# Kernel optimization log

Measured on AMD Instinct MI355X. Metric: run time of the kernel, lower is better.

## Reference

```python
import jax, jax.numpy as jnp
import numpy as np

N = 100            # node_num
B = 8              # batch
H = 256            # node_feature_hidden_dim
FD, FL = 16, 16    # node_feature_dim, node_feature_len
OUT = 4            # edge_output_dim
E = N * (N - 1)    # 9900 directed edges (off-diagonal)
_off = np.ones((N, N)) - np.eye(N)
REC, SEND = np.where(_off)   # rel_rec one-hot rows = REC, rel_send = SEND
REC = jnp.asarray(REC, jnp.int32)
SEND = jnp.asarray(SEND, jnp.int32)
BN_EPS = 1e-5


def _mlp(x, w1, b1, w2, b2, g, beta):
    # Linear-ReLU-Linear-ReLU-BatchNorm1d (training-mode batch stats, dropout=0)
    h = jax.nn.relu(x @ w1 + b1)
    h = jax.nn.relu(h @ w2 + b2)
    b_, e_, f_ = h.shape
    hf = h.reshape(b_ * e_, f_)
    mu = hf.mean(0)
    var = hf.var(0)  # biased variance, as torch BN uses for normalization
    hn = (hf - mu) * jax.lax.rsqrt(var + BN_EPS) * g + beta
    return hn.reshape(b_, e_, f_)


def _node2edge(x):
    # gather form of rel_send @ x / rel_rec @ x, cat([senders, receivers])
    return jnp.concatenate([x[:, SEND, :], x[:, REC, :]], axis=2)


def _edge2node(x):
    # scatter form of rel_rec.T @ x; original divides by incoming.size(1) == N
    incoming = jnp.zeros((x.shape[0], N, x.shape[2]), x.dtype).at[:, REC, :].add(x)
    return incoming / N


def setup_inputs() -> dict:
    key = jax.random.key(0)
    ks = jax.random.split(key, 40)

    def rn(k, shape, s=0.05):
        return (jax.random.normal(k, shape) * s).astype(jnp.float32)

    inp = {
        'x': rn(ks[0], (B, N, FD, FL), 1.0),
        'h': rn(ks[1], (B, N, 8, 8), 1.0),
        't_nodes': N,
        't_edges': E,
        'nodes_mask': jnp.ones((N,), jnp.int32),
        'edges_mask': jnp.ones((E,), jnp.int32),
    }
    n_in = {'mlp1': FD * FL, 'mlp2': 2 * H, 'mlp3': H, 'mlp4': 3 * H}
    i = 2
    for name, nin in n_in.items():
        inp[name + '_w1'] = rn(ks[i], (nin, H)); i += 1
        inp[name + '_b1'] = jnp.full((H,), 0.1, jnp.float32)
        inp[name + '_w2'] = rn(ks[i], (H, H)); i += 1
        inp[name + '_b2'] = jnp.full((H,), 0.1, jnp.float32)
        inp[name + '_g'] = jnp.ones((H,), jnp.float32)
        inp[name + '_beta'] = jnp.zeros((H,), jnp.float32)
    inp['fc_w'] = rn(ks[i], (H, OUT)); i += 1
    inp['fc_b'] = jnp.full((OUT,), 0.1, jnp.float32)
    return inp


def reference(x, h, t_nodes, t_edges, nodes_mask, edges_mask,
              mlp1_w1, mlp1_b1, mlp1_w2, mlp1_b2, mlp1_g, mlp1_beta,
              mlp2_w1, mlp2_b1, mlp2_w2, mlp2_b2, mlp2_g, mlp2_beta,
              mlp3_w1, mlp3_b1, mlp3_w2, mlp3_b2, mlp3_g, mlp3_beta,
              mlp4_w1, mlp4_b1, mlp4_w2, mlp4_b2, mlp4_g, mlp4_beta,
              fc_w, fc_b):
    # h, t_nodes, t_edges, nodes_mask, edges_mask are unused by the original forward
    xx = x.reshape(x.shape[0], x.shape[1], -1).astype(jnp.float32)  # [B,N,FD*FL]
    xx = _mlp(xx, mlp1_w1, mlp1_b1, mlp1_w2, mlp1_b2, mlp1_g, mlp1_beta)  # [B,N,H]
    xe = _node2edge(xx)                                                   # [B,E,2H]
    xe = _mlp(xe, mlp2_w1, mlp2_b1, mlp2_w2, mlp2_b2, mlp2_g, mlp2_beta)  # [B,E,H]
    x_skip = xe
    xn = _edge2node(xe)                                                   # [B,N,H]
    xn = _mlp(xn, mlp3_w1, mlp3_b1, mlp3_w2, mlp3_b2, mlp3_g, mlp3_beta)
    xe2 = _node2edge(xn)                                                  # [B,E,2H]
    xc = jnp.concatenate([xe2, x_skip], axis=2)                           # [B,E,3H]
    xc = _mlp(xc, mlp4_w1, mlp4_b1, mlp4_w2, mlp4_b2, mlp4_g, mlp4_beta)  # [B,E,H]
    z_g = xc @ fc_w + fc_b                                                # [B,E,OUT]
    return z_g
```

## Files before the change

kernel.cpp:

```cpp
#include <hip/hip_runtime.h>
#include <hip/hip_bf16.h>

#define Nn 100
#define Bb 8
#define Hh 256
#define Ee 9900
#define RE 79200
#define RN 800
#define BN_EPS 1e-5f

typedef __attribute__((ext_vector_type(8))) unsigned short ushort8_t;
typedef __attribute__((ext_vector_type(4))) unsigned short ushort4_t;
typedef __attribute__((ext_vector_type(8))) short bf16x8;
typedef __attribute__((ext_vector_type(4))) float f32x4;

__device__ __forceinline__ float bf2f(unsigned short u){
  return __uint_as_float(((unsigned)u) << 16);
}
__device__ __forceinline__ unsigned short f2bf(float f){
  unsigned u = __float_as_uint(f);
  return (unsigned short)((u + 0x7fffu + ((u >> 16) & 1u)) >> 16);
}

__device__ __forceinline__ void affine_prologue(const float* __restrict__ stats,
    float cnt, const float* __restrict__ g, const float* __restrict__ beta,
    float* a, float* c, int tid){
  if (tid < 256){
    float inv = 1.0f / cnt;
    float mu  = stats[tid] * inv;
    float var = fmaxf(stats[256 + tid] * inv - mu * mu, 0.f);
    float aa  = g[tid] * rsqrtf(var + BN_EPS);
    a[tid] = aa;
    c[tid] = beta[tid] - mu * aa;
  }
}

__device__ __forceinline__ void affine_reg(const float* __restrict__ stats,
    float cnt, const float* __restrict__ g, const float* __restrict__ be,
    int cb, float4& av, float4& cv){
  float4 s = *(const float4*)(stats + cb);
  float4 q = *(const float4*)(stats + 256 + cb);
  float4 gg = *(const float4*)(g + cb);
  float4 bb = *(const float4*)(be + cb);
  float inv = 1.0f / cnt;
  float mx = s.x*inv, my = s.y*inv, mz = s.z*inv, mw = s.w*inv;
  av.x = gg.x * rsqrtf(fmaxf(q.x*inv - mx*mx, 0.f) + BN_EPS); cv.x = bb.x - mx*av.x;
  av.y = gg.y * rsqrtf(fmaxf(q.y*inv - my*my, 0.f) + BN_EPS); cv.y = bb.y - my*av.y;
  av.z = gg.z * rsqrtf(fmaxf(q.z*inv - mz*mz, 0.f) + BN_EPS); cv.z = bb.z - mz*av.z;
  av.w = gg.w * rsqrtf(fmaxf(q.w*inv - mw*mw, 0.f) + BN_EPS); cv.w = bb.w - mw*av.w;
}

__device__ __forceinline__ void gemm_f32(const float* IN, const float* __restrict__ W,
                                         float acc[8][4], int tr, int tc){
  for (int k = 0; k < 256; k += 4){
    float4 w0 = *(const float4*)(W + (size_t)(k+0)*256 + 4*tc);
    float4 w1 = *(const float4*)(W + (size_t)(k+1)*256 + 4*tc);
    float4 w2 = *(const float4*)(W + (size_t)(k+2)*256 + 4*tc);
    float4 w3 = *(const float4*)(W + (size_t)(k+3)*256 + 4*tc);
    #pragma unroll
    for (int rr = 0; rr < 8; rr++){
      float4 iv = *(const float4*)(IN + (tr*8+rr)*256 + k);
      acc[rr][0] += iv.x*w0.x + iv.y*w1.x + iv.z*w2.x + iv.w*w3.x;
      acc[rr][1] += iv.x*w0.y + iv.y*w1.y + iv.z*w2.y + iv.w*w3.y;
      acc[rr][2] += iv.x*w0.z + iv.y*w1.z + iv.z*w2.z + iv.w*w3.z;
      acc[rr][3] += iv.x*w0.w + iv.y*w1.w + iv.z*w2.w + iv.w*w3.w;
    }
  }
}

template<int KW>
__device__ __forceinline__ void mfma_gemm(const unsigned short* Alds,
    const unsigned short* __restrict__ Bf, f32x4 acc[2][4], int w, int lane){
  const int l15 = lane & 15, kg = lane >> 4;
  for (int ks = 0; ks < KW/32; ks++){
    int byte0 = ((l15*KW      + ks*32 + kg*8) * 2) ^ ((l15 & 7) << 4);
    int byte1 = (((16+l15)*KW + ks*32 + kg*8) * 2) ^ ((l15 & 7) << 4);
    bf16x8 a0 = *(const bf16x8*)((const char*)Alds + byte0);
    bf16x8 a1 = *(const bf16x8*)((const char*)Alds + byte1);
    const unsigned short* bp = Bf + ((size_t)(ks*16 + w*4)*64 + lane)*8;
    #pragma unroll
    for (int cf = 0; cf < 4; cf++){
      bf16x8 b = *(const bf16x8*)(bp + cf*64*8);
      acc[0][cf] = __builtin_amdgcn_mfma_f32_16x16x32_bf16(a0, b, acc[0][cf], 0,0,0);
      acc[1][cf] = __builtin_amdgcn_mfma_f32_16x16x32_bf16(a1, b, acc[1][cf], 0,0,0);
    }
  }
}

__device__ __forceinline__ void zero_acc(f32x4 acc[2][4]){
  #pragma unroll
  for (int i = 0; i < 2; i++)
    #pragma unroll
    for (int j = 0; j < 4; j++){
      f32x4 z = {0.f, 0.f, 0.f, 0.f};
      acc[i][j] = z;
    }
}

#define STATS_PUSH(statsp)                                   \
  __syncthreads();                                           \
  atomicAdd(&(statsp)[tid], red[tid]);                       \
  atomicAdd(&(statsp)[tid + 256], red[tid + 256]);

__global__ void k_wprep(const float* __restrict__ W, unsigned short* __restrict__ out,
                        int ktiles){
  int id = blockIdx.x * 256 + threadIdx.x;
  int total = ktiles * 16 * 64;
  if (id >= total) return;
  int lane = id & 63, tile = id >> 6;
  int tc = tile & 15, tk = tile >> 4;
  int kbase = tk*32 + (lane>>4)*8, col = tc*16 + (lane&15);
  ushort8_t o;
  #pragma unroll
  for (int j = 0; j < 8; j++) o[j] = f2bf(W[(size_t)(kbase+j)*256 + col]);
  *(ushort8_t*)(out + (size_t)id*8) = o;
}

__global__ __launch_bounds__(256,2) void k_mlp1(
    const float* __restrict__ x,
    const float* __restrict__ W1, const float* __restrict__ b1,
    const float* __restrict__ W2, const float* __restrict__ b2,
    float* __restrict__ h1, float* __restrict__ stats){
  __shared__ float IN[32*256];
  __shared__ float O1[32*256];
  __shared__ float red[512];
  int tid = threadIdx.x, tr = tid >> 6, tc = tid & 63;
  int r0 = blockIdx.x * 32;
  #pragma unroll
  for (int j = 0; j < 8; j++){
    int idx = tid*4 + j*1024;
    *(float4*)(IN + idx) = *(const float4*)(x + (size_t)r0*256 + idx);
  }
  red[tid] = 0.f; red[tid + 256] = 0.f;
  __syncthreads();
  float acc[8][4];
  #pragma unroll
  for (int rr = 0; rr < 8; rr++){ acc[rr][0]=acc[rr][1]=acc[rr][2]=acc[rr][3]=0.f; }
  gemm_f32(IN, W1, acc, tr, tc);
  {
    float4 bb = *(const float4*)(b1 + 4*tc);
    #pragma unroll
    for (int rr = 0; rr < 8; rr++){
      float4 o;
      o.x = fmaxf(acc[rr][0]+bb.x, 0.f);
      o.y = fmaxf(acc[rr][1]+bb.y, 0.f);
      o.z = fmaxf(acc[rr][2]+bb.z, 0.f);
      o.w = fmaxf(acc[rr][3]+bb.w, 0.f);
      *(float4*)(O1 + (tr*8+rr)*256 + 4*tc) = o;
    }
  }
  __syncthreads();
  #pragma unroll
  for (int rr = 0; rr < 8; rr++){ acc[rr][0]=acc[rr][1]=acc[rr][2]=acc[rr][3]=0.f; }
  gemm_f32(O1, W2, acc, tr, tc);
  {
    float4 bb = *(const float4*)(b2 + 4*tc);
    float ls0=0,ls1=0,ls2=0,ls3=0,lq0=0,lq1=0,lq2=0,lq3=0;
    #pragma unroll
    for (int rr = 0; rr < 8; rr++){
      float4 v;
      v.x = fmaxf(acc[rr][0]+bb.x, 0.f);
      v.y = fmaxf(acc[rr][1]+bb.y, 0.f);
      v.z = fmaxf(acc[rr][2]+bb.z, 0.f);
      v.w = fmaxf(acc[rr][3]+bb.w, 0.f);
      *(float4*)(h1 + ((size_t)(r0 + tr*8 + rr))*256 + 4*tc) = v;
      ls0+=v.x; lq0+=v.x*v.x; ls1+=v.y; lq1+=v.y*v.y;
      ls2+=v.z; lq2+=v.z*v.z; ls3+=v.w; lq3+=v.w*v.w;
    }
    atomicAdd(&red[4*tc+0], ls0); atomicAdd(&red[4*tc+1], ls1);
    atomicAdd(&red[4*tc+2], ls2); atomicAdd(&red[4*tc+3], ls3);
    atomicAdd(&red[256+4*tc+0], lq0); atomicAdd(&red[256+4*tc+1], lq1);
    atomicAdd(&red[256+4*tc+2], lq2); atomicAdd(&red[256+4*tc+3], lq3);
  }
  STATS_PUSH(stats)
}

__global__ __launch_bounds__(256,4) void k_mlp2(
    const float* __restrict__ h1, const float* __restrict__ stats1,
    const float* __restrict__ g1, const float* __restrict__ be1,
    const unsigned short* __restrict__ W1f, const float* __restrict__ b1,
    const unsigned short* __restrict__ W2f, const float* __restrict__ b2,
    unsigned short* __restrict__ h2, float* __restrict__ stats2){
  __shared__ unsigned short A[32*512];
  __shared__ float red[512];
  int tid = threadIdx.x, w = tid >> 6, lane = tid & 63;
  int l15 = lane & 15, kg = lane >> 4;
  int r0 = blockIdx.x * 32;
  red[tid] = 0.f; red[tid + 256] = 0.f;
  {
    int cb = (lane & 31) * 8, half = lane >> 5;
    float4 a0, c0, a1, c1;
    affine_reg(stats1, (float)RN, g1, be1, cb,     a0, c0);
    affine_reg(stats1, (float)RN, g1, be1, cb + 4, a1, c1);
    #pragma unroll
    for (int rr = 0; rr < 8; rr++){
      int rl = w*8+rr, rg = r0 + rl;
      int b = rg / Ee, e = rg - b*Ee;
      int i = e / 99, kk = e - i*99;
      int snd = kk + (kk >= i);
      int node = half ? i : snd;
      const float* sp = h1 + ((size_t)(b*Nn + node))*256 + cb;
      float4 v0 = *(const float4*)sp, v1 = *(const float4*)(sp+4);
      ushort8_t o;
      o[0]=f2bf(v0.x*a0.x+c0.x); o[1]=f2bf(v0.y*a0.y+c0.y);
      o[2]=f2bf(v0.z*a0.z+c0.z); o[3]=f2bf(v0.w*a0.w+c0.w);
      o[4]=f2bf(v1.x*a1.x+c1.x); o[5]=f2bf(v1.y*a1.y+c1.y);
      o[6]=f2bf(v1.z*a1.z+c1.z); o[7]=f2bf(v1.w*a1.w+c1.w);
      int byte = ((rl*512 + half*256 + cb)*2) ^ ((rl&7)<<4);
      *(ushort8_t*)((char*)A + byte) = o;
    }
  }
  __syncthreads();
  f32x4 acc[2][4];
  zero_acc(acc);
  mfma_gemm<512>(A, W1f, acc, w, lane);
  __syncthreads();
  unsigned short* O1 = A;
  {
    #pragma unroll
    for (int cf = 0; cf < 4; cf++){
      int col = w*64 + cf*16 + l15;
      float bb = b1[col];
      #pragma unroll
      for (int rf = 0; rf < 2; rf++){
        #pragma unroll
        for (int r = 0; r < 4; r++){
          int row = rf*16 + kg*4 + r;
          float v = fmaxf(acc[rf][cf][r] + bb, 0.f);
          int byte = ((row*256 + col)*2) ^ ((row&7)<<4);
          *(unsigned short*)((char*)O1 + byte) = f2bf(v);
        }
      }
    }
  }
  __syncthreads();
  f32x4 acc2[2][4];
  zero_acc(acc2);
  mfma_gemm<256>(O1, W2f, acc2, w, lane);
  {
    #pragma unroll
    for (int cf = 0; cf < 4; cf++){
      int col = w*64 + cf*16 + l15;
      float bb = b2[col];
      float ls = 0.f, lq = 0.f;
      #pragma unroll
      for (int rf = 0; rf < 2; rf++){
        #pragma unroll
        for (int r = 0; r < 4; r++){
          int row = rf*16 + kg*4 + r;
          float v = fmaxf(acc2[rf][cf][r] + bb, 0.f);
          h2[(size_t)(r0 + row)*256 + col] = f2bf(v);
          ls += v; lq += v*v;
        }
      }
      atomicAdd(&red[col], ls);
      atomicAdd(&red[256+col], lq);
    }
  }
  STATS_PUSH(stats2)
}

__global__ __launch_bounds__(256,4) void k_e2n(
    const unsigned short* __restrict__ h2, float* __restrict__ h3in){
  int m = blockIdx.x;
  int b = m / Nn, i = m - b*Nn;
  int c = threadIdx.x;
  const unsigned short* base = h2 + ((size_t)(b*Ee + i*99))*256 + c;
  float s = 0.f;
  #pragma unroll 4
  for (int j = 0; j < 99; j++) s += bf2f(base[(size_t)j*256]);
  h3in[(size_t)m*256 + c] = s;
}

__global__ __launch_bounds__(256,2) void k_mlp3(
    const float* __restrict__ h3in, const float* __restrict__ stats2,
    const float* __restrict__ g2, const float* __restrict__ be2,
    const float* __restrict__ W1, const float* __restrict__ b1,
    const float* __restrict__ W2, const float* __restrict__ b2,
    float* __restrict__ h3, float* __restrict__ stats3){
  __shared__ float IN[32*256];
  __shared__ float O1[32*256];
  __shared__ float red[512];
  __shared__ float ap[256], cp[256];
  int tid = threadIdx.x, tr = tid >> 6, lane = tid & 63, tc = lane;
  int r0 = blockIdx.x * 32;
  affine_prologue(stats2, (float)RE, g2, be2, ap, cp, tid);
  red[tid] = 0.f; red[tid + 256] = 0.f;
  __syncthreads();
  {
    int cb = lane * 4;
    float4 av = *(const float4*)(ap+cb), cv = *(const float4*)(cp+cb);
    #pragma unroll
    for (int rr = 0; rr < 8; rr++){
      int m = r0 + tr*8 + rr;
      float4 s = *(const float4*)(h3in + (size_t)m*256 + cb);
      float4 o;
      o.x = (s.x*av.x + 99.f*cv.x) * 0.01f;
      o.y = (s.y*av.y + 99.f*cv.y) * 0.01f;
      o.z = (s.z*av.z + 99.f*cv.z) * 0.01f;
      o.w = (s.w*av.w + 99.f*cv.w) * 0.01f;
      *(float4*)(IN + (tr*8+rr)*256 + cb) = o;
    }
  }
  __syncthreads();
  float acc[8][4];
  #pragma unroll
  for (int rr = 0; rr < 8; rr++){ acc[rr][0]=acc[rr][1]=acc[rr][2]=acc[rr][3]=0.f; }
  gemm_f32(IN, W1, acc, tr, tc);
  {
    float4 bb = *(const float4*)(b1 + 4*tc);
    #pragma unroll
    for (int rr = 0; rr < 8; rr++){
      float4 o;
      o.x = fmaxf(acc[rr][0]+bb.x, 0.f);
      o.y = fmaxf(acc[rr][1]+bb.y, 0.f);
      o.z = fmaxf(acc[rr][2]+bb.z, 0.f);
      o.w = fmaxf(acc[rr][3]+bb.w, 0.f);
      *(float4*)(O1 + (tr*8+rr)*256 + 4*tc) = o;
    }
  }
  __syncthreads();
  #pragma unroll
  for (int rr = 0; rr < 8; rr++){ acc[rr][0]=acc[rr][1]=acc[rr][2]=acc[rr][3]=0.f; }
  gemm_f32(O1, W2, acc, tr, tc);
  {
    float4 bb = *(const float4*)(b2 + 4*tc);
    float ls0=0,ls1=0,ls2=0,ls3=0,lq0=0,lq1=0,lq2=0,lq3=0;
    #pragma unroll
    for (int rr = 0; rr < 8; rr++){
      float4 v;
      v.x = fmaxf(acc[rr][0]+bb.x, 0.f);
      v.y = fmaxf(acc[rr][1]+bb.y, 0.f);
      v.z = fmaxf(acc[rr][2]+bb.z, 0.f);
      v.w = fmaxf(acc[rr][3]+bb.w, 0.f);
      *(float4*)(h3 + ((size_t)(r0 + tr*8 + rr))*256 + 4*tc) = v;
      ls0+=v.x; lq0+=v.x*v.x; ls1+=v.y; lq1+=v.y*v.y;
      ls2+=v.z; lq2+=v.z*v.z; ls3+=v.w; lq3+=v.w*v.w;
    }
    atomicAdd(&red[4*tc+0], ls0); atomicAdd(&red[4*tc+1], ls1);
    atomicAdd(&red[4*tc+2], ls2); atomicAdd(&red[4*tc+3], ls3);
    atomicAdd(&red[256+4*tc+0], lq0); atomicAdd(&red[256+4*tc+1], lq1);
    atomicAdd(&red[256+4*tc+2], lq2); atomicAdd(&red[256+4*tc+3], lq3);
  }
  STATS_PUSH(stats3)
}

__global__ __launch_bounds__(256,3) void k_mlp4(
    const float* __restrict__ h3, const unsigned short* __restrict__ h2,
    const float* __restrict__ stats3, const float* __restrict__ g3, const float* __restrict__ be3,
    const float* __restrict__ stats2, const float* __restrict__ g2, const float* __restrict__ be2,
    const unsigned short* __restrict__ W1f, const float* __restrict__ b1,
    const unsigned short* __restrict__ W2f, const float* __restrict__ b2,
    unsigned short* __restrict__ h4, float* __restrict__ stats4){
  __shared__ unsigned short A[32*768];
  __shared__ float red[512];
  int tid = threadIdx.x, w = tid >> 6, lane = tid & 63;
  int l15 = lane & 15, kg = lane >> 4;
  int r0 = blockIdx.x * 32;
  red[tid] = 0.f; red[tid + 256] = 0.f;
  {
    int cb = (lane & 31) * 8, half = lane >> 5;
    float4 a0, c0, a1, c1;
    affine_reg(stats3, (float)RN, g3, be3, cb,     a0, c0);
    affine_reg(stats3, (float)RN, g3, be3, cb + 4, a1, c1);
    #pragma unroll
    for (int rr = 0; rr < 8; rr++){
      int rl = w*8+rr, rg = r0 + rl;
      int b = rg / Ee, e = rg - b*Ee;
      int i = e / 99, kk = e - i*99;
      int snd = kk + (kk >= i);
      int node = half ? i : snd;
      const float* sp = h3 + ((size_t)(b*Nn + node))*256 + cb;
      float4 v0 = *(const float4*)sp, v1 = *(const float4*)(sp+4);
      ushort8_t o;
      o[0]=f2bf(v0.x*a0.x+c0.x); o[1]=f2bf(v0.y*a0.y+c0.y);
      o[2]=f2bf(v0.z*a0.z+c0.z); o[3]=f2bf(v0.w*a0.w+c0.w);
      o[4]=f2bf(v1.x*a1.x+c1.x); o[5]=f2bf(v1.y*a1.y+c1.y);
      o[6]=f2bf(v1.z*a1.z+c1.z); o[7]=f2bf(v1.w*a1.w+c1.w);
      int byte = ((rl*768 + half*256 + cb)*2) ^ ((rl&7)<<4);
      *(ushort8_t*)((char*)A + byte) = o;
    }
  }
  {
    int cb = lane * 4;
    float4 av, cv;
    affine_reg(stats2, (float)RE, g2, be2, cb, av, cv);
    #pragma unroll
    for (int rr = 0; rr < 8; rr++){
      int rl = w*8+rr, rg = r0 + rl;
      ushort4_t hv = *(const ushort4_t*)(h2 + (size_t)rg*256 + cb);
      ushort4_t o;
      o[0]=f2bf(bf2f(hv[0])*av.x+cv.x);
      o[1]=f2bf(bf2f(hv[1])*av.y+cv.y);
      o[2]=f2bf(bf2f(hv[2])*av.z+cv.z);
      o[3]=f2bf(bf2f(hv[3])*av.w+cv.w);
      int byte = ((rl*768 + 512 + cb)*2) ^ ((rl&7)<<4);
      *(ushort4_t*)((char*)A + byte) = o;
    }
  }
  __syncthreads();
  f32x4 acc[2][4];
  zero_acc(acc);
  mfma_gemm<768>(A, W1f, acc, w, lane);
  __syncthreads();
  unsigned short* O1 = A;
  {
    #pragma unroll
    for (int cf = 0; cf < 4; cf++){
      int col = w*64 + cf*16 + l15;
      float bb = b1[col];
      #pragma unroll
      for (int rf = 0; rf < 2; rf++){
        #pragma unroll
        for (int r = 0; r < 4; r++){
          int row = rf*16 + kg*4 + r;
          float v = fmaxf(acc[rf][cf][r] + bb, 0.f);
          int byte = ((row*256 + col)*2) ^ ((row&7)<<4);
          *(unsigned short*)((char*)O1 + byte) = f2bf(v);
        }
      }
    }
  }
  __syncthreads();
  f32x4 acc2[2][4];
  zero_acc(acc2);
  mfma_gemm<256>(O1, W2f, acc2, w, lane);
  {
    #pragma unroll
    for (int cf = 0; cf < 4; cf++){
      int col = w*64 + cf*16 + l15;
      float bb = b2[col];
      float ls = 0.f, lq = 0.f;
      #pragma unroll
      for (int rf = 0; rf < 2; rf++){
        #pragma unroll
        for (int r = 0; r < 4; r++){
          int row = rf*16 + kg*4 + r;
          float v = fmaxf(acc2[rf][cf][r] + bb, 0.f);
          h4[(size_t)(r0 + row)*256 + col] = f2bf(v);
          ls += v; lq += v*v;
        }
      }
      atomicAdd(&red[col], ls);
      atomicAdd(&red[256+col], lq);
    }
  }
  STATS_PUSH(stats4)
}

__global__ __launch_bounds__(256,2) void k_out(
    const unsigned short* __restrict__ h4, const float* __restrict__ stats4,
    const float* __restrict__ g4, const float* __restrict__ be4,
    const float* __restrict__ fcw, const float* __restrict__ fcb,
    float* __restrict__ out){
  __shared__ unsigned short T[64*264];
  __shared__ float a4[256], c4[256], Wl[1024];
  int tid = threadIdx.x;
  affine_prologue(stats4, (float)RE, g4, be4, a4, c4, tid);
  #pragma unroll
  for (int j = 0; j < 4; j++){ int id = tid + j*256; Wl[id] = fcw[id]; }
  int r0 = blockIdx.x * 64;
  #pragma unroll
  for (int j = 0; j < 8; j++){
    int flat = tid + j*256;
    int rl = flat >> 5, cs = (flat & 31) * 8;
    ushort8_t v = {0,0,0,0,0,0,0,0};
    if (r0 + rl < RE) v = *(const ushort8_t*)(h4 + (size_t)(r0+rl)*256 + cs);
    *(ushort8_t*)(&T[rl*264 + cs]) = v;
  }
  __syncthreads();
  int row = tid >> 2, o = tid & 3;
  if (r0 + row < RE){
    float acc = fcb[o];
    for (int k = 0; k < 256; k += 8){
      ushort8_t iv = *(const ushort8_t*)(&T[row*264 + k]);
      #pragma unroll
      for (int kk = 0; kk < 8; kk++){
        float v = bf2f(iv[kk]) * a4[k+kk] + c4[k+kk];
        acc += v * Wl[(k+kk)*4 + o];
      }
    }
    out[(size_t)(r0+row)*4 + o] = acc;
  }
}

extern "C" void kernel_launch(void* const* d_in, const int* in_sizes, int n_in,
                              void* d_out, int out_size, void* d_ws, size_t ws_size,
                              hipStream_t stream){
  const float* x    = (const float*)d_in[0];
  const float* m1w1 = (const float*)d_in[6];  const float* m1b1 = (const float*)d_in[7];
  const float* m1w2 = (const float*)d_in[8];  const float* m1b2 = (const float*)d_in[9];
  const float* m1g  = (const float*)d_in[10]; const float* m1be = (const float*)d_in[11];
  const float* m2w1 = (const float*)d_in[12]; const float* m2b1 = (const float*)d_in[13];
  const float* m2w2 = (const float*)d_in[14]; const float* m2b2 = (const float*)d_in[15];
  const float* m2g  = (const float*)d_in[16]; const float* m2be = (const float*)d_in[17];
  const float* m3w1 = (const float*)d_in[18]; const float* m3b1 = (const float*)d_in[19];
  const float* m3w2 = (const float*)d_in[20]; const float* m3b2 = (const float*)d_in[21];
  const float* m3g  = (const float*)d_in[22]; const float* m3be = (const float*)d_in[23];
  const float* m4w1 = (const float*)d_in[24]; const float* m4b1 = (const float*)d_in[25];
  const float* m4w2 = (const float*)d_in[26]; const float* m4b2 = (const float*)d_in[27];
  const float* m4g  = (const float*)d_in[28]; const float* m4be = (const float*)d_in[29];
  const float* fcw  = (const float*)d_in[30]; const float* fcb  = (const float*)d_in[31];

  size_t need_bytes = (204800ull*3 + 2048ull) * 4ull
                    + 2ull * (size_t)RE * 256ull * 2ull
                    + 458752ull * 2ull;
  if (ws_size < need_bytes) return;

  float* ws = (float*)d_ws;
  float* h1   = ws;
  float* h3   = ws + 204800;
  float* stats= ws + 409600;
  float* h3in = ws + 411648;
  unsigned short* h2 = (unsigned short*)(ws + 616448);
  unsigned short* h4 = h2 + (size_t)RE * 256;
  unsigned short* w2a = h4 + (size_t)RE * 256;
  unsigned short* w2b = w2a + 512*256;
  unsigned short* w4a = w2b + 256*256;
  unsigned short* w4b = w4a + 768*256;

  hipMemsetAsync(stats, 0, 2048 * sizeof(float), stream);

  k_wprep<<<(16*16*64)/256, 256, 0, stream>>>(m2w1, w2a, 16);
  k_wprep<<<( 8*16*64)/256, 256, 0, stream>>>(m2w2, w2b, 8);
  k_wprep<<<(24*16*64)/256, 256, 0, stream>>>(m4w1, w4a, 24);
  k_wprep<<<( 8*16*64)/256, 256, 0, stream>>>(m4w2, w4b, 8);

  k_mlp1<<<RN/32, 256, 0, stream>>>(x, m1w1, m1b1, m1w2, m1b2, h1, stats);
  k_mlp2<<<RE/32, 256, 0, stream>>>(h1, stats, m1g, m1be,
                                    w2a, m2b1, w2b, m2b2, h2, stats + 512);
  k_e2n<<<RN, 256, 0, stream>>>(h2, h3in);
  k_mlp3<<<RN/32, 256, 0, stream>>>(h3in, stats + 512, m2g, m2be,
                                    m3w1, m3b1, m3w2, m3b2, h3, stats + 1024);
  k_mlp4<<<RE/32, 256, 0, stream>>>(h3, h2, stats + 1024, m3g, m3be,
                                    stats + 512, m2g, m2be,
                                    w4a, m4b1, w4b, m4b2, h4, stats + 1536);
  k_out<<<(RE+63)/64, 256, 0, stream>>>(h4, stats + 1536, m4g, m4be,
                                        fcw, fcb, (float*)d_out);
}
```

Measured before the change: 478.6 us.

## Factor edge first-layer GEMMs into per-node projections gathered per edge

Because each edge input is a concatenation of sender and receiver node features, the first linear layer of MLP2 and the node part of MLP4 are rewritten as per-node products P = x·W_send and Q = x·W_recv. A new k_nodepq kernel computes these in fp32 on 800 node rows, and the edge kernels gather P[sender] + Q[receiver] instead of running a K=512 (or the node part of K=768) GEMM over 79200 edge rows. This removes most of the first-layer edge FLOPs and the smaller shared-memory tiles allow higher occupancy. The cost is two extra small launches, extra fp32 gather traffic, and a different rounding path (fp32 node products instead of a bf16 MFMA over the concatenated input).

Measured after the change: 513.9 us. 1.07x slower.

```diff
diff --git a/kernel.cpp b/kernel.cpp
--- a/kernel.cpp
+++ b/kernel.cpp
@@ -175,62 +175,70 @@
   STATS_PUSH(stats)
 }
 
-__global__ __launch_bounds__(256,4) void k_mlp2(
-    const float* __restrict__ h1, const float* __restrict__ stats1,
-    const float* __restrict__ g1, const float* __restrict__ be1,
-    const unsigned short* __restrict__ W1f, const float* __restrict__ b1,
+__global__ __launch_bounds__(256,2) void k_nodepq(
+    const float* __restrict__ hsrc, const float* __restrict__ stats,
+    const float* __restrict__ g, const float* __restrict__ be,
+    const float* __restrict__ W512,
+    float* __restrict__ P, float* __restrict__ Q){
+  __shared__ float IN[32*256];
+  int tid = threadIdx.x, tr = tid >> 6, tc = tid & 63;
+  int part = blockIdx.x / 25;
+  int r0 = (blockIdx.x % 25) * 32;
+  int cb = (tid*4) & 255;
+  float4 av, cv;
+  affine_reg(stats, (float)RN, g, be, cb, av, cv);
+  #pragma unroll
+  for (int j = 0; j < 8; j++){
+    int idx = tid*4 + j*1024;
+    int row = idx >> 8;
+    float4 v = *(const float4*)(hsrc + (size_t)(r0+row)*256 + cb);
+    float4 o;
+    o.x = v.x*av.x + cv.x; o.y = v.y*av.y + cv.y;
+    o.z = v.z*av.z + cv.z; o.w = v.w*av.w + cv.w;
+    *(float4*)(IN + idx) = o;
+  }
+  __syncthreads();
+  float acc[8][4];
+  #pragma unroll
+  for (int rr = 0; rr < 8; rr++){ acc[rr][0]=acc[rr][1]=acc[rr][2]=acc[rr][3]=0.f; }
+  gemm_f32(IN, W512 + (size_t)part*65536, acc, tr, tc);
+  float* out = part ? Q : P;
+  #pragma unroll
+  for (int rr = 0; rr < 8; rr++){
+    float4 o; o.x=acc[rr][0]; o.y=acc[rr][1]; o.z=acc[rr][2]; o.w=acc[rr][3];
+    *(float4*)(out + (size_t)(r0 + tr*8 + rr)*256 + 4*tc) = o;
+  }
+}
+
+__global__ __launch_bounds__(256,6) void k_mlp2(
+    const float* __restrict__ P2, const float* __restrict__ Q2,
+    const float* __restrict__ b1,
     const unsigned short* __restrict__ W2f, const float* __restrict__ b2,
     unsigned short* __restrict__ h2, float* __restrict__ stats2){
-  __shared__ unsigned short A[32*512];
+  __shared__ unsigned short O1[32*256];
   __shared__ float red[512];
   int tid = threadIdx.x, w = tid >> 6, lane = tid & 63;
   int l15 = lane & 15, kg = lane >> 4;
   int r0 = blockIdx.x * 32;
   red[tid] = 0.f; red[tid + 256] = 0.f;
   {
-    int cb = (lane & 31) * 8, half = lane >> 5;
-    float4 a0, c0, a1, c1;
-    affine_reg(stats1, (float)RN, g1, be1, cb,     a0, c0);
-    affine_reg(stats1, (float)RN, g1, be1, cb + 4, a1, c1);
+    int cb = lane * 4;
+    float4 bb = *(const float4*)(b1 + cb);
     #pragma unroll
     for (int rr = 0; rr < 8; rr++){
       int rl = w*8+rr, rg = r0 + rl;
       int b = rg / Ee, e = rg - b*Ee;
       int i = e / 99, kk = e - i*99;
       int snd = kk + (kk >= i);
-      int node = half ? i : snd;
-      const float* sp = h1 + ((size_t)(b*Nn + node))*256 + cb;
-      float4 v0 = *(const float4*)sp, v1 = *(const float4*)(sp+4);
-      ushort8_t o;
-      o[0]=f2bf(v0.x*a0.x+c0.x); o[1]=f2bf(v0.y*a0.y+c0.y);
-      o[2]=f2bf(v0.z*a0.z+c0.z); o[3]=f2bf(v0.w*a0.w+c0.w);
-      o[4]=f2bf(v1.x*a1.x+c1.x); o[5]=f2bf(v1.y*a1.y+c1.y);
-      o[6]=f2bf(v1.z*a1.z+c1.z); o[7]=f2bf(v1.w*a1.w+c1.w);
-      int byte = ((rl*512 + half*256 + cb)*2) ^ ((rl&7)<<4);
-      *(ushort8_t*)((char*)A + byte) = o;
-    }
-  }
-  __syncthreads();
-  f32x4 acc[2][4];
-  zero_acc(acc);
-  mfma_gemm<512>(A, W1f, acc, w, lane);
-  __syncthreads();
-  unsigned short* O1 = A;
-  {
-    #pragma unroll
-    for (int cf = 0; cf < 4; cf++){
-      int col = w*64 + cf*16 + l15;
-      float bb = b1[col];
-      #pragma unroll
-      for (int rf = 0; rf < 2; rf++){
-        #pragma unroll
-        for (int r = 0; r < 4; r++){
-          int row = rf*16 + kg*4 + r;
-          float v = fmaxf(acc[rf][cf][r] + bb, 0.f);
-          int byte = ((row*256 + col)*2) ^ ((row&7)<<4);
-          *(unsigned short*)((char*)O1 + byte) = f2bf(v);
-        }
-      }
+      float4 pv = *(const float4*)(P2 + ((size_t)(b*Nn + snd))*256 + cb);
+      float4 qv = *(const float4*)(Q2 + ((size_t)(b*Nn + i))*256 + cb);
+      ushort4_t o;
+      o[0] = f2bf(fmaxf(pv.x+qv.x+bb.x, 0.f));
+      o[1] = f2bf(fmaxf(pv.y+qv.y+bb.y, 0.f));
+      o[2] = f2bf(fmaxf(pv.z+qv.z+bb.z, 0.f));
+      o[3] = f2bf(fmaxf(pv.w+qv.w+bb.w, 0.f));
+      int byte = ((rl*256 + cb)*2) ^ ((rl&7)<<4);
+      *(ushort4_t*)((char*)O1 + byte) = o;
     }
   }
   __syncthreads();
@@ -345,41 +353,28 @@
   STATS_PUSH(stats3)
 }
 
-__global__ __launch_bounds__(256,3) void k_mlp4(
-    const float* __restrict__ h3, const unsigned short* __restrict__ h2,
-    const float* __restrict__ stats3, const float* __restrict__ g3, const float* __restrict__ be3,
+__global__ __launch_bounds__(256,6) void k_mlp4(
+    const unsigned short* __restrict__ h2,
     const float* __restrict__ stats2, const float* __restrict__ g2, const float* __restrict__ be2,
-    const unsigned short* __restrict__ W1f, const float* __restrict__ b1,
+    const float* __restrict__ P4, const float* __restrict__ Q4,
+    const float* __restrict__ b1,
+    const unsigned short* __restrict__ Wsf,
     const unsigned short* __restrict__ W2f, const float* __restrict__ b2,
     unsigned short* __restrict__ h4, float* __restrict__ stats4){
-  __shared__ unsigned short A[32*768];
+  __shared__ unsigned short A[32*256];
   __shared__ float red[512];
+  __shared__ int sIdx[32], rIdx[32];
   int tid = threadIdx.x, w = tid >> 6, lane = tid & 63;
   int l15 = lane & 15, kg = lane >> 4;
   int r0 = blockIdx.x * 32;
   red[tid] = 0.f; red[tid + 256] = 0.f;
-  {
-    int cb = (lane & 31) * 8, half = lane >> 5;
-    float4 a0, c0, a1, c1;
-    affine_reg(stats3, (float)RN, g3, be3, cb,     a0, c0);
-    affine_reg(stats3, (float)RN, g3, be3, cb + 4, a1, c1);
-    #pragma unroll
-    for (int rr = 0; rr < 8; rr++){
-      int rl = w*8+rr, rg = r0 + rl;
-      int b = rg / Ee, e = rg - b*Ee;
-      int i = e / 99, kk = e - i*99;
-      int snd = kk + (kk >= i);
-      int node = half ? i : snd;
-      const float* sp = h3 + ((size_t)(b*Nn + node))*256 + cb;
-      float4 v0 = *(const float4*)sp, v1 = *(const float4*)(sp+4);
-      ushort8_t o;
-      o[0]=f2bf(v0.x*a0.x+c0.x); o[1]=f2bf(v0.y*a0.y+c0.y);
-      o[2]=f2bf(v0.z*a0.z+c0.z); o[3]=f2bf(v0.w*a0.w+c0.w);
-      o[4]=f2bf(v1.x*a1.x+c1.x); o[5]=f2bf(v1.y*a1.y+c1.y);
-      o[6]=f2bf(v1.z*a1.z+c1.z); o[7]=f2bf(v1.w*a1.w+c1.w);
-      int byte = ((rl*768 + half*256 + cb)*2) ^ ((rl&7)<<4);
-      *(ushort8_t*)((char*)A + byte) = o;
-    }
+  if (tid < 32){
+    int rg = r0 + tid;
+    int b = rg / Ee, e = rg - b*Ee;
+    int i = e / 99, kk = e - i*99;
+    int snd = kk + (kk >= i);
+    sIdx[tid] = (b*Nn + snd)*256;
+    rIdx[tid] = (b*Nn + i)*256;
   }
   {
     int cb = lane * 4;
@@ -394,14 +389,14 @@
       o[1]=f2bf(bf2f(hv[1])*av.y+cv.y);
       o[2]=f2bf(bf2f(hv[2])*av.z+cv.z);
       o[3]=f2bf(bf2f(hv[3])*av.w+cv.w);
-      int byte = ((rl*768 + 512 + cb)*2) ^ ((rl&7)<<4);
+      int byte = ((rl*256 + cb)*2) ^ ((rl&7)<<4);
       *(ushort4_t*)((char*)A + byte) = o;
     }
   }
   __syncthreads();
   f32x4 acc[2][4];
   zero_acc(acc);
-  mfma_gemm<768>(A, W1f, acc, w, lane);
+  mfma_gemm<256>(A, Wsf, acc, w, lane);
   __syncthreads();
   unsigned short* O1 = A;
   {
@@ -414,7 +409,8 @@
         #pragma unroll
         for (int r = 0; r < 4; r++){
           int row = rf*16 + kg*4 + r;
-          float v = fmaxf(acc[rf][cf][r] + bb, 0.f);
+          float v = acc[rf][cf][r] + P4[sIdx[row] + col] + Q4[rIdx[row] + col] + bb;
+          v = fmaxf(v, 0.f);
           int byte = ((row*256 + col)*2) ^ ((row&7)<<4);
           *(unsigned short*)((char*)O1 + byte) = f2bf(v);
         }
@@ -502,9 +498,8 @@
   const float* m4g  = (const float*)d_in[28]; const float* m4be = (const float*)d_in[29];
   const float* fcw  = (const float*)d_in[30]; const float* fcb  = (const float*)d_in[31];
 
-  size_t need_bytes = (204800ull*3 + 2048ull) * 4ull
-                    + 2ull * (size_t)RE * 256ull * 2ull
-                    + 458752ull * 2ull;
+  size_t need_bytes = 1435648ull * 4ull
+                    + (2ull * (size_t)RE * 256ull + 3ull * 65536ull) * 2ull;
   if (ws_size < need_bytes) return;
 
   float* ws = (float*)d_ws;
@@ -512,29 +507,31 @@
   float* h3   = ws + 204800;
   float* stats= ws + 409600;
   float* h3in = ws + 411648;
-  unsigned short* h2 = (unsigned short*)(ws + 616448);
-  unsigned short* h4 = h2 + (size_t)RE * 256;
-  unsigned short* w2a = h4 + (size_t)RE * 256;
-  unsigned short* w2b = w2a + 512*256;
-  unsigned short* w4a = w2b + 256*256;
-  unsigned short* w4b = w4a + 768*256;
+  float* P2   = ws + 616448;
+  float* Q2   = ws + 821248;
+  float* P4   = ws + 1026048;
+  float* Q4   = ws + 1230848;
+  unsigned short* h2  = (unsigned short*)(ws + 1435648);
+  unsigned short* h4  = h2 + (size_t)RE * 256;
+  unsigned short* w2b = h4 + (size_t)RE * 256;
+  unsigned short* w4s = w2b + 65536;
+  unsigned short* w4b = w4s + 65536;
 
   hipMemsetAsync(stats, 0, 2048 * sizeof(float), stream);
 
-  k_wprep<<<(16*16*64)/256, 256, 0, stream>>>(m2w1, w2a, 16);
-  k_wprep<<<( 8*16*64)/256, 256, 0, stream>>>(m2w2, w2b, 8);
-  k_wprep<<<(24*16*64)/256, 256, 0, stream>>>(m4w1, w4a, 24);
-  k_wprep<<<( 8*16*64)/256, 256, 0, stream>>>(m4w2, w4b, 8);
+  k_wprep<<<(8*16*64)/256, 256, 0, stream>>>(m2w2, w2b, 8);
+  k_wprep<<<(8*16*64)/256, 256, 0, stream>>>(m4w1 + (size_t)512*256, w4s, 8);
+  k_wprep<<<(8*16*64)/256, 256, 0, stream>>>(m4w2, w4b, 8);
 
   k_mlp1<<<RN/32, 256, 0, stream>>>(x, m1w1, m1b1, m1w2, m1b2, h1, stats);
-  k_mlp2<<<RE/32, 256, 0, stream>>>(h1, stats, m1g, m1be,
-                                    w2a, m2b1, w2b, m2b2, h2, stats + 512);
+  k_nodepq<<<50, 256, 0, stream>>>(h1, stats, m1g, m1be, m2w1, P2, Q2);
+  k_mlp2<<<RE/32, 256, 0, stream>>>(P2, Q2, m2b1, w2b, m2b2, h2, stats + 512);
   k_e2n<<<RN, 256, 0, stream>>>(h2, h3in);
   k_mlp3<<<RN/32, 256, 0, stream>>>(h3in, stats + 512, m2g, m2be,
                                     m3w1, m3b1, m3w2, m3b2, h3, stats + 1024);
-  k_mlp4<<<RE/32, 256, 0, stream>>>(h3, h2, stats + 1024, m3g, m3be,
-                                    stats + 512, m2g, m2be,
-                                    w4a, m4b1, w4b, m4b2, h4, stats + 1536);
+  k_nodepq<<<50, 256, 0, stream>>>(h3, stats + 1024, m3g, m3be, m4w1, P4, Q4);
+  k_mlp4<<<RE/32, 256, 0, stream>>>(h2, stats + 512, m2g, m2be,
+                                    P4, Q4, m4b1, w4s, w4b, m4b2, h4, stats + 1536);
   k_out<<<(RE+63)/64, 256, 0, stream>>>(h4, stats + 1536, m4g, m4be,
                                         fcw, fcb, (float*)d_out);
 }
```

## Split K-dimension staging into 256-wide chunks to shrink LDS and raise occupancy

Applied to the files above, without the earlier changes.

The edge MLP kernels (mlp2, mlp4) now stage the concatenated input in 256-column chunks and accumulate the first GEMM across parts, instead of staging the full 512/768-wide row tile at once. This cuts shared memory per block to 16KB plus reduction space, and launch bounds are raised to 6 blocks per CU to exploit that. The cost is extra barriers per part and less latency hiding within each block, since gather loads and MFMA no longer overlap across parts. Correctness depends on the packed weight layout placing each 256-row K slice at a 65536-element offset.

After: 597.9 us. 1.25x slower.

```diff
diff --git a/kernel.cpp b/kernel.cpp
--- a/kernel.cpp
+++ b/kernel.cpp
@@ -68,13 +68,12 @@
   }
 }
 
-template<int KW>
-__device__ __forceinline__ void mfma_gemm(const unsigned short* Alds,
+__device__ __forceinline__ void mfma_gemm256(const unsigned short* Alds,
     const unsigned short* __restrict__ Bf, f32x4 acc[2][4], int w, int lane){
   const int l15 = lane & 15, kg = lane >> 4;
-  for (int ks = 0; ks < KW/32; ks++){
-    int byte0 = ((l15*KW      + ks*32 + kg*8) * 2) ^ ((l15 & 7) << 4);
-    int byte1 = (((16+l15)*KW + ks*32 + kg*8) * 2) ^ ((l15 & 7) << 4);
+  for (int ks = 0; ks < 8; ks++){
+    int byte0 = ((l15*256      + ks*32 + kg*8) * 2) ^ ((l15 & 7) << 4);
+    int byte1 = (((16+l15)*256 + ks*32 + kg*8) * 2) ^ ((l15 & 7) << 4);
     bf16x8 a0 = *(const bf16x8*)((const char*)Alds + byte0);
     bf16x8 a1 = *(const bf16x8*)((const char*)Alds + byte1);
     const unsigned short* bp = Bf + ((size_t)(ks*16 + w*4)*64 + lane)*8;
@@ -175,47 +174,43 @@
   STATS_PUSH(stats)
 }
 
-__global__ __launch_bounds__(256,4) void k_mlp2(
+__global__ __launch_bounds__(256,6) void k_mlp2(
     const float* __restrict__ h1, const float* __restrict__ stats1,
     const float* __restrict__ g1, const float* __restrict__ be1,
-    const unsigned short* __restrict__ W1f, const float* __restrict__ b1,
+    const unsigned short* __restrict__ W1f,
+    const float* __restrict__ b1,
     const unsigned short* __restrict__ W2f, const float* __restrict__ b2,
     unsigned short* __restrict__ h2, float* __restrict__ stats2){
-  __shared__ unsigned short A[32*512];
+  __shared__ unsigned short A[32*256];
   __shared__ float red[512];
   int tid = threadIdx.x, w = tid >> 6, lane = tid & 63;
   int l15 = lane & 15, kg = lane >> 4;
   int r0 = blockIdx.x * 32;
   red[tid] = 0.f; red[tid + 256] = 0.f;
-  {
-    int cb = (lane & 31) * 8, half = lane >> 5;
-    float4 a0, c0, a1, c1;
-    affine_reg(stats1, (float)RN, g1, be1, cb,     a0, c0);
-    affine_reg(stats1, (float)RN, g1, be1, cb + 4, a1, c1);
+  int cb = lane * 4;
+  float4 av, cv;
+  affine_reg(stats1, (float)RN, g1, be1, cb, av, cv);
+  f32x4 acc[2][4];
+  zero_acc(acc);
+  for (int part = 0; part < 2; part++){
     #pragma unroll
     for (int rr = 0; rr < 8; rr++){
       int rl = w*8+rr, rg = r0 + rl;
       int b = rg / Ee, e = rg - b*Ee;
       int i = e / 99, kk = e - i*99;
       int snd = kk + (kk >= i);
-      int node = half ? i : snd;
-      const float* sp = h1 + ((size_t)(b*Nn + node))*256 + cb;
-      float4 v0 = *(const float4*)sp, v1 = *(const float4*)(sp+4);
-      ushort8_t o;
-      o[0]=f2bf(v0.x*a0.x+c0.x); o[1]=f2bf(v0.y*a0.y+c0.y);
-      o[2]=f2bf(v0.z*a0.z+c0.z); o[3]=f2bf(v0.w*a0.w+c0.w);
-      o[4]=f2bf(v1.x*a1.x+c1.x); o[5]=f2bf(v1.y*a1.y+c1.y);
-      o[6]=f2bf(v1.z*a1.z+c1.z); o[7]=f2bf(v1.w*a1.w+c1.w);
-      int byte = ((rl*512 + half*256 + cb)*2) ^ ((rl&7)<<4);
-      *(ushort8_t*)((char*)A + byte) = o;
-    }
-  }
-  __syncthreads();
-  f32x4 acc[2][4];
-  zero_acc(acc);
-  mfma_gemm<512>(A, W1f, acc, w, lane);
-  __syncthreads();
-  unsigned short* O1 = A;
+      int node = part ? i : snd;
+      float4 v = *(const float4*)(h1 + ((size_t)(b*Nn + node))*256 + cb);
+      ushort4_t o;
+      o[0]=f2bf(v.x*av.x+cv.x); o[1]=f2bf(v.y*av.y+cv.y);
+      o[2]=f2bf(v.z*av.z+cv.z); o[3]=f2bf(v.w*av.w+cv.w);
+      int byte = ((rl*256 + cb)*2) ^ ((rl&7)<<4);
+      *(ushort4_t*)((char*)A + byte) = o;
+    }
+    __syncthreads();
+    mfma_gemm256(A, W1f + (size_t)part*65536, acc, w, lane);
+    __syncthreads();
+  }
   {
     #pragma unroll
     for (int cf = 0; cf < 4; cf++){
@@ -228,7 +223,7 @@
           int row = rf*16 + kg*4 + r;
           float v = fmaxf(acc[rf][cf][r] + bb, 0.f);
           int byte = ((row*256 + col)*2) ^ ((row&7)<<4);
-          *(unsigned short*)((char*)O1 + byte) = f2bf(v);
+          *(unsigned short*)((char*)A + byte) = f2bf(v);
         }
       }
     }
@@ -236,7 +231,7 @@
   __syncthreads();
   f32x4 acc2[2][4];
   zero_acc(acc2);
-  mfma_gemm<256>(O1, W2f, acc2, w, lane);
+  mfma_gemm256(A, W2f, acc2, w, lane);
   {
     #pragma unroll
     for (int cf = 0; cf < 4; cf++){
@@ -345,65 +340,53 @@
   STATS_PUSH(stats3)
 }
 
-__global__ __launch_bounds__(256,3) void k_mlp4(
+__global__ __launch_bounds__(256,6) void k_mlp4(
     const float* __restrict__ h3, const unsigned short* __restrict__ h2,
     const float* __restrict__ stats3, const float* __restrict__ g3, const float* __restrict__ be3,
     const float* __restrict__ stats2, const float* __restrict__ g2, const float* __restrict__ be2,
-    const unsigned short* __restrict__ W1f, const float* __restrict__ b1,
+    const unsigned short* __restrict__ W1f,
+    const float* __restrict__ b1,
     const unsigned short* __restrict__ W2f, const float* __restrict__ b2,
     unsigned short* __restrict__ h4, float* __restrict__ stats4){
-  __shared__ unsigned short A[32*768];
+  __shared__ unsigned short A[32*256];
   __shared__ float red[512];
   int tid = threadIdx.x, w = tid >> 6, lane = tid & 63;
   int l15 = lane & 15, kg = lane >> 4;
   int r0 = blockIdx.x * 32;
   red[tid] = 0.f; red[tid + 256] = 0.f;
-  {
-    int cb = (lane & 31) * 8, half = lane >> 5;
-    float4 a0, c0, a1, c1;
-    affine_reg(stats3, (float)RN, g3, be3, cb,     a0, c0);
-    affine_reg(stats3, (float)RN, g3, be3, cb + 4, a1, c1);
-    #pragma unroll
-    for (int rr = 0; rr < 8; rr++){
-      int rl = w*8+rr, rg = r0 + rl;
-      int b = rg / Ee, e = rg - b*Ee;
-      int i = e / 99, kk = e - i*99;
-      int snd = kk + (kk >= i);
-      int node = half ? i : snd;
-      const float* sp = h3 + ((size_t)(b*Nn + node))*256 + cb;
-      float4 v0 = *(const float4*)sp, v1 = *(const float4*)(sp+4);
-      ushort8_t o;
-      o[0]=f2bf(v0.x*a0.x+c0.x); o[1]=f2bf(v0.y*a0.y+c0.y);
-      o[2]=f2bf(v0.z*a0.z+c0.z); o[3]=f2bf(v0.w*a0.w+c0.w);
-      o[4]=f2bf(v1.x*a1.x+c1.x); o[5]=f2bf(v1.y*a1.y+c1.y);
-      o[6]=f2bf(v1.z*a1.z+c1.z); o[7]=f2bf(v1.w*a1.w+c1.w);
-      int byte = ((rl*768 + half*256 + cb)*2) ^ ((rl&7)<<4);
-      *(ushort8_t*)((char*)A + byte) = o;
-    }
-  }
-  {
-    int cb = lane * 4;
-    float4 av, cv;
-    affine_reg(stats2, (float)RE, g2, be2, cb, av, cv);
-    #pragma unroll
-    for (int rr = 0; rr < 8; rr++){
-      int rl = w*8+rr, rg = r0 + rl;
-      ushort4_t hv = *(const ushort4_t*)(h2 + (size_t)rg*256 + cb);
-      ushort4_t o;
-      o[0]=f2bf(bf2f(hv[0])*av.x+cv.x);
-      o[1]=f2bf(bf2f(hv[1])*av.y+cv.y);
-      o[2]=f2bf(bf2f(hv[2])*av.z+cv.z);
-      o[3]=f2bf(bf2f(hv[3])*av.w+cv.w);
-      int byte = ((rl*768 + 512 + cb)*2) ^ ((rl&7)<<4);
-      *(ushort4_t*)((char*)A + byte) = o;
-    }
-  }
-  __syncthreads();
+  int cb = lane * 4;
+  float4 a3v, c3v, a2v, c2v;
+  affine_reg(stats3, (float)RN, g3, be3, cb, a3v, c3v);
+  affine_reg(stats2, (float)RE, g2, be2, cb, a2v, c2v);
   f32x4 acc[2][4];
   zero_acc(acc);
-  mfma_gemm<768>(A, W1f, acc, w, lane);
-  __syncthreads();
-  unsigned short* O1 = A;
+  for (int part = 0; part < 3; part++){
+    #pragma unroll
+    for (int rr = 0; rr < 8; rr++){
+      int rl = w*8+rr, rg = r0 + rl;
+      ushort4_t o;
+      if (part < 2){
+        int b = rg / Ee, e = rg - b*Ee;
+        int i = e / 99, kk = e - i*99;
+        int snd = kk + (kk >= i);
+        int node = part ? i : snd;
+        float4 v = *(const float4*)(h3 + ((size_t)(b*Nn + node))*256 + cb);
+        o[0]=f2bf(v.x*a3v.x+c3v.x); o[1]=f2bf(v.y*a3v.y+c3v.y);
+        o[2]=f2bf(v.z*a3v.z+c3v.z); o[3]=f2bf(v.w*a3v.w+c3v.w);
+      } else {
+        ushort4_t hv = *(const ushort4_t*)(h2 + (size_t)rg*256 + cb);
+        o[0]=f2bf(bf2f(hv[0])*a2v.x+c2v.x);
+        o[1]=f2bf(bf2f(hv[1])*a2v.y+c2v.y);
+        o[2]=f2bf(bf2f(hv[2])*a2v.z+c2v.z);
+        o[3]=f2bf(bf2f(hv[3])*a2v.w+c2v.w);
+      }
+      int byte = ((rl*256 + cb)*2) ^ ((rl&7)<<4);
+      *(ushort4_t*)((char*)A + byte) = o;
+    }
+    __syncthreads();
+    mfma_gemm256(A, W1f + (size_t)part*65536, acc, w, lane);
+    __syncthreads();
+  }
   {
     #pragma unroll
     for (int cf = 0; cf < 4; cf++){
@@ -416,7 +399,7 @@
           int row = rf*16 + kg*4 + r;
           float v = fmaxf(acc[rf][cf][r] + bb, 0.f);
           int byte = ((row*256 + col)*2) ^ ((row&7)<<4);
-          *(unsigned short*)((char*)O1 + byte) = f2bf(v);
+          *(unsigned short*)((char*)A + byte) = f2bf(v);
         }
       }
     }
@@ -424,7 +407,7 @@
   __syncthreads();
   f32x4 acc2[2][4];
   zero_acc(acc2);
-  mfma_gemm<256>(O1, W2f, acc2, w, lane);
+  mfma_gemm256(A, W2f, acc2, w, lane);
   {
     #pragma unroll
     for (int cf = 0; cf < 4; cf++){
```
